# Kernel tuning notes

Measured on AMD Instinct MI355X. Metric: run time of the kernel, lower is better.

## Reference

```python
import jax, jax.numpy as jnp
import numpy as np

N, E, IN, H, O, K = 50000, 800000, 256, 128, 32, 5
ALPHA, EPS = 0.1, 1e-5


def setup_inputs() -> dict:
    key = jax.random.key(0)
    ks = jax.random.split(key, 20)
    nrm = lambda k, shape, s=0.02: jax.random.normal(k, shape, dtype=jnp.float32) * s
    H2 = H // 2
    return {
        "x": jax.random.normal(ks[0], (N, IN), dtype=jnp.float32),
        "edge_index": jax.random.randint(ks[1], (2, E), 0, N),
        "edge_weight": jax.random.uniform(ks[2], (E,), dtype=jnp.float32),
        # lin1 + bn1
        "W1": nrm(ks[3], (IN, H)), "b1": jnp.zeros((H,), jnp.float32),
        "g1": jnp.ones((H,), jnp.float32), "be1": jnp.zeros((H,), jnp.float32),
        "m1": nrm(ks[4], (H,), 0.1), "v1": 1.0 + 0.1 * jax.random.uniform(ks[5], (H,), dtype=jnp.float32),
        # lin2 + bn2
        "W2": nrm(ks[6], (H, H)), "b2": jnp.zeros((H,), jnp.float32),
        "g2": jnp.ones((H,), jnp.float32), "be2": jnp.zeros((H,), jnp.float32),
        "m2": nrm(ks[7], (H,), 0.1), "v2": 1.0 + 0.1 * jax.random.uniform(ks[8], (H,), dtype=jnp.float32),
        # attention over hop outputs (K+1)
        "att": jnp.ones((K + 1,), jnp.float32) + nrm(ks[9], (K + 1,), 0.1),
        # head: Linear(H, H//2) + BN + ReLU + Linear(H//2, O)
        "W3": nrm(ks[10], (H, H2)), "b3": jnp.zeros((H2,), jnp.float32),
        "g3": jnp.ones((H2,), jnp.float32), "be3": jnp.zeros((H2,), jnp.float32),
        "m3": nrm(ks[11], (H2,), 0.1), "v3": 1.0 + 0.1 * jax.random.uniform(ks[12], (H2,), dtype=jnp.float32),
        "W4": nrm(ks[13], (H2, O)), "b4": jnp.zeros((O,), jnp.float32),
    }


def _bn(t, g, b, m, v):
    # eval-mode BatchNorm1d using running stats
    return (t - m) * (g / jnp.sqrt(v + EPS)) + b


def reference(x, edge_index, edge_weight, W1, b1, g1, be1, m1, v1,
              W2, b2, g2, be2, m2, v2, att,
              W3, b3, g3, be3, m3, v3, W4, b4):
    n = x.shape[0]
    row, col = edge_index[0], edge_index[1]

    h = jax.nn.relu(_bn(x @ W1 + b1, g1, be1, m1, v1))
    identity = h
    h = jax.nn.relu(_bn(h @ W2 + b2, g2, be2, m2, v2)) + identity

    # weighted edge normalization: out-weight sum per source node, clamped >= 1
    wsum = jnp.maximum(jax.ops.segment_sum(edge_weight, row, num_segments=n), 1.0)
    edge_norm = edge_weight / wsum[row]  # [E]

    def prop(h_in):
        # APPNP-style: K inner iterations blending toward this call's h0
        h0 = h_in
        hk = h_in
        for _ in range(K):
            msg = hk[row] * edge_norm[:, None]          # [E, H] gather + scale
            agg = jax.ops.segment_sum(msg, col, num_segments=n)  # scatter-add
            hk = (1.0 - ALPHA) * agg + ALPHA * h0
        return hk

    xs = [h]
    hc = h
    for _ in range(K):  # outer loop: att has K+1 weights
        hc = prop(hc)
        xs.append(hc)

    stacked = jnp.stack(xs, axis=-1)          # [N, H, K+1]
    w = jax.nn.softmax(att)                   # [K+1]
    fused = jnp.einsum('nhk,k->nh', stacked, w)

    hid = jax.nn.relu(_bn(fused @ W3 + b3, g3, be3, m3, v3))
    return hid @ W4 + b4
```

## Files before the change

kernel.cpp:

```cpp
#include <hip/hip_runtime.h>
#include <cstddef>
#include <cstdint>

namespace {

constexpr int N   = 50000;
constexpr int E   = 800000;
constexpr int IN  = 256;
constexpr int H   = 128;
constexpr int H2v = 64;
constexpr int O   = 32;
constexpr int K   = 5;
constexpr float ALPHA = 0.1f;
constexpr float EPS   = 1e-5f;
constexpr int SCAN_CH = 1024;
constexpr int SCAN_NB = (N + SCAN_CH - 1) / SCAN_CH;
constexpr int NPAD = 50048;
constexpr int NPW  = 8;

typedef __bf16 bf16x8 __attribute__((ext_vector_type(8)));
typedef float  f32x4  __attribute__((ext_vector_type(4)));

__device__ inline uint32_t pack2_bf16(float x, float y) {
  uint32_t ux = __float_as_uint(x);
  uint32_t uy = __float_as_uint(y);
  ux = (ux + 0x7FFFu + ((ux >> 16) & 1u)) >> 16;
  uy = (uy + 0x7FFFu + ((uy >> 16) & 1u)) & 0xFFFF0000u;
  return uy | ux;
}
__device__ inline unsigned short bf16_1(float x) {
  uint32_t u = __float_as_uint(x);
  return (unsigned short)((u + 0x7FFFu + ((u >> 16) & 1u)) >> 16);
}
__device__ inline float bf16_lo(uint32_t v) { return __uint_as_float(v << 16); }
__device__ inline float bf16_hi(uint32_t v) { return __uint_as_float(v & 0xFFFF0000u); }
__device__ inline float bf16_f(unsigned short h) { return __uint_as_float(((uint32_t)h) << 16); }

__global__ void zero2_kernel(int* __restrict__ a, int* __restrict__ b, int n) {
  int i = blockIdx.x * blockDim.x + threadIdx.x;
  if (i < n) { a[i] = 0; b[i] = 0; }
}

__global__ void softmax_att_kernel(const float* __restrict__ att, float* __restrict__ wk) {
  if (threadIdx.x == 0 && blockIdx.x == 0) {
    float mx = att[0];
    for (int i = 1; i < K + 1; ++i) mx = fmaxf(mx, att[i]);
    float ex[K + 1];
    float s = 0.f;
    for (int i = 0; i < K + 1; ++i) { ex[i] = expf(att[i] - mx); s += ex[i]; }
    for (int i = 0; i < K + 1; ++i) wk[i] = ex[i] / s;
  }
}

__global__ void hist_kernel(const int* __restrict__ row, const int* __restrict__ col,
                            const float* __restrict__ ew,
                            int* __restrict__ deg, float* __restrict__ wsum) {
  int i = blockIdx.x * blockDim.x + threadIdx.x;
  if (i < E) {
    atomicAdd(&deg[col[i]], 1);
    atomicAdd(&wsum[row[i]], ew[i]);
  }
}

__global__ __launch_bounds__(256) void scan_local_kernel(const int* __restrict__ deg,
                                                         int* __restrict__ offs,
                                                         int* __restrict__ bsum) {
  __shared__ int sd[256];
  int base = blockIdx.x * SCAN_CH;
  int t = threadIdx.x;
  int v[4];
  int s = 0;
#pragma unroll
  for (int u = 0; u < 4; ++u) {
    int i = base + t * 4 + u;
    v[u] = (i < N) ? deg[i] : 0;
    s += v[u];
  }
  sd[t] = s;
  __syncthreads();
  int val = s;
  for (int off = 1; off < 256; off <<= 1) {
    int x = (t >= off) ? sd[t - off] : 0;
    __syncthreads();
    val += x;
    sd[t] = val;
    __syncthreads();
  }
  int excl = val - s;
#pragma unroll
  for (int u = 0; u < 4; ++u) {
    int i = base + t * 4 + u;
    if (i < N) offs[i] = excl;
    excl += v[u];
  }
  if (t == 255) bsum[blockIdx.x] = val;
}

__global__ void scan_bsum_kernel(int* __restrict__ bsum) {
  if (threadIdx.x == 0 && blockIdx.x == 0) {
    int acc = 0;
    for (int i = 0; i < SCAN_NB; ++i) {
      int v = bsum[i];
      bsum[i] = acc;
      acc += v;
    }
    bsum[SCAN_NB] = acc;
  }
}

__global__ void scan_add_kernel(int* __restrict__ offs, const int* __restrict__ bsum,
                                int* __restrict__ cursor) {
  int i = blockIdx.x * blockDim.x + threadIdx.x;
  if (i < N) {
    int o = offs[i] + bsum[i / SCAN_CH];
    offs[i] = o;
    cursor[i] = o;
  }
  if (i == 0) offs[N] = bsum[SCAN_NB];
}

__global__ void fill_kernel(const int* __restrict__ row, const int* __restrict__ col,
                            const float* __restrict__ ew, const float* __restrict__ wsum,
                            int* __restrict__ cursor, uint2* __restrict__ csr) {
  int i = blockIdx.x * blockDim.x + threadIdx.x;
  if (i < E) {
    int d = col[i];
    int p = atomicAdd(&cursor[d], 1);
    int s = row[i];
    float w = ew[i] / fmaxf(wsum[s], 1.0f);
    csr[p] = make_uint2((uint32_t)s, __float_as_uint(w));
  }
}

__global__ void conv_x_kernel(const float* __restrict__ x, unsigned short* __restrict__ xbf) {
  int i = blockIdx.x * blockDim.x + threadIdx.x;
  size_t base = (size_t)i * 8;
  int r = (int)(base / IN);
  uint4 pk = {0, 0, 0, 0};
  if (r < N) {
    float4 a = *(const float4*)&x[base];
    float4 b = *(const float4*)&x[base + 4];
    pk.x = pack2_bf16(a.x, a.y);
    pk.y = pack2_bf16(a.z, a.w);
    pk.z = pack2_bf16(b.x, b.y);
    pk.w = pack2_bf16(b.z, b.w);
  }
  *(uint4*)&xbf[base] = pk;
}

__global__ void conv_wt_kernel(const float* __restrict__ W, unsigned short* __restrict__ Wt,
                               int Kdim) {
  int t = blockIdx.x * blockDim.x + threadIdx.x;
  int k8 = Kdim / 8;
  int n = t / k8;
  int kk = (t % k8) * 8;
  if (n >= H) return;
  float f[8];
#pragma unroll
  for (int j = 0; j < 8; ++j) f[j] = W[(size_t)(kk + j) * H + n];
  uint4 pk;
  pk.x = pack2_bf16(f[0], f[1]);
  pk.y = pack2_bf16(f[2], f[3]);
  pk.z = pack2_bf16(f[4], f[5]);
  pk.w = pack2_bf16(f[6], f[7]);
  *(uint4*)&Wt[(size_t)n * Kdim + kk] = pk;
}

__global__ __launch_bounds__(256) void mlp1_mfma_kernel(
    const unsigned short* __restrict__ xbf, const unsigned short* __restrict__ Wt1,
    const float* __restrict__ b1, const float* __restrict__ g1,
    const float* __restrict__ be1, const float* __restrict__ m1,
    const float* __restrict__ v1, unsigned short* __restrict__ h1bf) {
  int wave = threadIdx.x >> 6;
  int lane = threadIdx.x & 63;
  int m_base = blockIdx.x * 64 + wave * 16;
  int idx16 = lane & 15;
  int quad = lane >> 4;
  bf16x8 afrag[8];
  const unsigned short* xrow = xbf + (size_t)(m_base + idx16) * IN + quad * 8;
#pragma unroll
  for (int k0 = 0; k0 < 8; ++k0) afrag[k0] = *(const bf16x8*)(xrow + k0 * 32);
#pragma unroll
  for (int n0 = 0; n0 < 8; ++n0) {
    f32x4 acc = {0.f, 0.f, 0.f, 0.f};
    const unsigned short* wrow = Wt1 + (size_t)(n0 * 16 + idx16) * IN + quad * 8;
#pragma unroll
    for (int k0 = 0; k0 < 8; ++k0) {
      bf16x8 bfrag = *(const bf16x8*)(wrow + k0 * 32);
      acc = __builtin_amdgcn_mfma_f32_16x16x32_bf16(afrag[k0], bfrag, acc, 0, 0, 0);
    }
    int n = n0 * 16 + idx16;
    float sc = g1[n] * rsqrtf(v1[n] + EPS);
    float ad = b1[n] - m1[n];
    float bb = be1[n];
#pragma unroll
    for (int r = 0; r < 4; ++r) {
      int m = m_base + quad * 4 + r;
      float val = fmaxf((acc[r] + ad) * sc + bb, 0.f);
      h1bf[(size_t)m * H + n] = bf16_1(val);
    }
  }
}

__global__ __launch_bounds__(256) void mlp2_mfma_kernel(
    const unsigned short* __restrict__ h1bf, const unsigned short* __restrict__ Wt2,
    const float* __restrict__ b2, const float* __restrict__ g2,
    const float* __restrict__ be2, const float* __restrict__ m2,
    const float* __restrict__ v2, unsigned short* __restrict__ h0bf,
    float* __restrict__ fused, const float* __restrict__ wk) {
  int wave = threadIdx.x >> 6;
  int lane = threadIdx.x & 63;
  int m_base = blockIdx.x * 64 + wave * 16;
  int idx16 = lane & 15;
  int quad = lane >> 4;
  bf16x8 afrag[4];
  const unsigned short* arow = h1bf + (size_t)(m_base + idx16) * H + quad * 8;
#pragma unroll
  for (int k0 = 0; k0 < 4; ++k0) afrag[k0] = *(const bf16x8*)(arow + k0 * 32);
  float w0 = wk[0];
#pragma unroll
  for (int n0 = 0; n0 < 8; ++n0) {
    f32x4 acc = {0.f, 0.f, 0.f, 0.f};
    const unsigned short* wrow = Wt2 + (size_t)(n0 * 16 + idx16) * H + quad * 8;
#pragma unroll
    for (int k0 = 0; k0 < 4; ++k0) {
      bf16x8 bfrag = *(const bf16x8*)(wrow + k0 * 32);
      acc = __builtin_amdgcn_mfma_f32_16x16x32_bf16(afrag[k0], bfrag, acc, 0, 0, 0);
    }
    int n = n0 * 16 + idx16;
    float sc = g2[n] * rsqrtf(v2[n] + EPS);
    float ad = b2[n] - m2[n];
    float bb = be2[n];
#pragma unroll
    for (int r = 0; r < 4; ++r) {
      int m = m_base + quad * 4 + r;
      if (m < N) {
        float idv = bf16_f(h1bf[(size_t)m * H + n]);
        float val = fmaxf((acc[r] + ad) * sc + bb, 0.f) + idv;
        h0bf[(size_t)m * H + n] = bf16_1(val);
        fused[(size_t)m * H + n] = w0 * val;
      }
    }
  }
}

__global__ __launch_bounds__(256) void prop_kernel(
    const unsigned short* __restrict__ hk, const unsigned short* __restrict__ h0,
    unsigned short* __restrict__ outb,
    const int* __restrict__ offs, const uint2* __restrict__ csr,
    float* __restrict__ fused, const float* __restrict__ wk, int wj) {
  int wave = threadIdx.x >> 6;
  int lane = threadIdx.x & 63;
  int node0 = (blockIdx.x * 4 + wave) * NPW;
  int c = lane * 2;
  float wj_w = (wj >= 0) ? wk[wj] : 0.f;
  for (int nn = 0; nn < NPW; ++nn) {
    int node = node0 + nn;
    if (node >= N) return;
    int beg = offs[node];
    int end = offs[node + 1];
    float ax = 0.f, ay = 0.f;
    int e = beg;
    for (; e + 8 <= end; e += 8) {
      uint2 ew[8];
#pragma unroll
      for (int u = 0; u < 8; ++u) ew[u] = csr[e + u];
      uint32_t v[8];
#pragma unroll
      for (int u = 0; u < 8; ++u) v[u] = *(const uint32_t*)&hk[(size_t)ew[u].x * H + c];
#pragma unroll
      for (int u = 0; u < 8; ++u) {
        float w = __uint_as_float(ew[u].y);
        ax += w * bf16_lo(v[u]);
        ay += w * bf16_hi(v[u]);
      }
    }
    for (; e + 4 <= end; e += 4) {
      uint2 ew[4];
#pragma unroll
      for (int u = 0; u < 4; ++u) ew[u] = csr[e + u];
      uint32_t v[4];
#pragma unroll
      for (int u = 0; u < 4; ++u) v[u] = *(const uint32_t*)&hk[(size_t)ew[u].x * H + c];
#pragma unroll
      for (int u = 0; u < 4; ++u) {
        float w = __uint_as_float(ew[u].y);
        ax += w * bf16_lo(v[u]);
        ay += w * bf16_hi(v[u]);
      }
    }
    for (; e < end; ++e) {
      uint2 ew = csr[e];
      float w = __uint_as_float(ew.y);
      uint32_t v = *(const uint32_t*)&hk[(size_t)ew.x * H + c];
      ax += w * bf16_lo(v);
      ay += w * bf16_hi(v);
    }
    size_t idx = (size_t)node * H + c;
    uint32_t hv = *(const uint32_t*)&h0[idx];
    float vx = (1.f - ALPHA) * ax + ALPHA * bf16_lo(hv);
    float vy = (1.f - ALPHA) * ay + ALPHA * bf16_hi(hv);
    *(uint32_t*)&outb[idx] = pack2_bf16(vx, vy);
    if (wj >= 0) {
      float2 f = *(float2*)&fused[idx];
      f.x += wj_w * vx;
      f.y += wj_w * vy;
      *(float2*)&fused[idx] = f;
    }
  }
}

__global__ __launch_bounds__(64) void head_kernel(
    const float* __restrict__ fused, const float* __restrict__ W3,
    const float* __restrict__ b3, const float* __restrict__ g3,
    const float* __restrict__ be3, const float* __restrict__ m3,
    const float* __restrict__ v3, const float* __restrict__ W4,
    const float* __restrict__ b4, float* __restrict__ out) {
  __shared__ float fl[16][H];
  __shared__ float hl[16][H2v];
  int node0 = blockIdx.x * 16;
  int t = threadIdx.x;
  for (int idx = t * 4; idx < 16 * H; idx += 64 * 4) {
    int r = idx >> 7, c = idx & (H - 1);
    *(float4*)&fl[r][c] = *(const float4*)&fused[(size_t)(node0 + r) * H + c];
  }
  __syncthreads();
  {
    int ng = t >> 4;
    int c0 = (t & 15) * 4;
    float acc[4][4];
#pragma unroll
    for (int a = 0; a < 4; ++a)
#pragma unroll
      for (int b = 0; b < 4; ++b) acc[a][b] = 0.f;
    for (int k = 0; k < H; k += 4) {
      float4 xv[4];
#pragma unroll
      for (int a = 0; a < 4; ++a) xv[a] = *(const float4*)&fl[ng * 4 + a][k];
      float4 wv[4];
#pragma unroll
      for (int j = 0; j < 4; ++j) wv[j] = *(const float4*)&W3[(size_t)(k + j) * H2v + c0];
#pragma unroll
      for (int a = 0; a < 4; ++a) {
        float xa0 = xv[a].x, xa1 = xv[a].y, xa2 = xv[a].z, xa3 = xv[a].w;
        acc[a][0] += xa0 * wv[0].x + xa1 * wv[1].x + xa2 * wv[2].x + xa3 * wv[3].x;
        acc[a][1] += xa0 * wv[0].y + xa1 * wv[1].y + xa2 * wv[2].y + xa3 * wv[3].y;
        acc[a][2] += xa0 * wv[0].z + xa1 * wv[1].z + xa2 * wv[2].z + xa3 * wv[3].z;
        acc[a][3] += xa0 * wv[0].w + xa1 * wv[1].w + xa2 * wv[2].w + xa3 * wv[3].w;
      }
    }
    float sc[4], ad[4], bb[4];
#pragma unroll
    for (int b = 0; b < 4; ++b) {
      int c = c0 + b;
      sc[b] = g3[c] * rsqrtf(v3[c] + EPS);
      ad[b] = b3[c] - m3[c];
      bb[b] = be3[c];
    }
#pragma unroll
    for (int a = 0; a < 4; ++a)
#pragma unroll
      for (int b = 0; b < 4; ++b)
        hl[ng * 4 + a][c0 + b] = fmaxf((acc[a][b] + ad[b]) * sc[b] + bb[b], 0.f);
  }
  __syncthreads();
  {
    int co = t & 31;
    int nh = t >> 5;
    float bias = b4[co];
#pragma unroll
    for (int a = 0; a < 8; ++a) {
      int nloc = nh * 8 + a;
      float accf = bias;
      for (int k = 0; k < H2v; k += 4) {
        float4 hv = *(const float4*)&hl[nloc][k];
        accf += hv.x * W4[(size_t)(k + 0) * O + co];
        accf += hv.y * W4[(size_t)(k + 1) * O + co];
        accf += hv.z * W4[(size_t)(k + 2) * O + co];
        accf += hv.w * W4[(size_t)(k + 3) * O + co];
      }
      out[(size_t)(node0 + nloc) * O + co] = accf;
    }
  }
}

}

extern "C" void kernel_launch(void* const* d_in, const int* in_sizes, int n_in,
                              void* d_out, int out_size, void* d_ws, size_t ws_size,
                              hipStream_t stream) {
  const float* x   = (const float*)d_in[0];
  const int*   ei  = (const int*)d_in[1];
  const float* ew  = (const float*)d_in[2];
  const float* W1  = (const float*)d_in[3];
  const float* b1  = (const float*)d_in[4];
  const float* g1  = (const float*)d_in[5];
  const float* be1 = (const float*)d_in[6];
  const float* m1  = (const float*)d_in[7];
  const float* v1  = (const float*)d_in[8];
  const float* W2  = (const float*)d_in[9];
  const float* b2  = (const float*)d_in[10];
  const float* g2  = (const float*)d_in[11];
  const float* be2 = (const float*)d_in[12];
  const float* m2  = (const float*)d_in[13];
  const float* v2  = (const float*)d_in[14];
  const float* att = (const float*)d_in[15];
  const float* W3  = (const float*)d_in[16];
  const float* b3  = (const float*)d_in[17];
  const float* g3  = (const float*)d_in[18];
  const float* be3 = (const float*)d_in[19];
  const float* m3  = (const float*)d_in[20];
  const float* v3  = (const float*)d_in[21];
  const float* W4  = (const float*)d_in[22];
  const float* b4  = (const float*)d_in[23];
  const int* row = ei;
  const int* col = ei + E;
  float* out = (float*)d_out;

  char* p = (char*)d_ws;
  auto carve = [&](size_t bytes) -> void* {
    void* q = (void*)p;
    p += (bytes + 255) & ~(size_t)255;
    return q;
  };
  int*   deg     = (int*)carve((size_t)N * 4);
  float* wsum    = (float*)carve((size_t)N * 4);
  int*   offs    = (int*)carve((size_t)(N + 1) * 4);
  int*   cursor  = (int*)carve((size_t)N * 4);
  int*   bsum    = (int*)carve((size_t)(SCAN_NB + 1) * 4);
  uint2* csr     = (uint2*)carve((size_t)E * 8);
  float* wk      = (float*)carve(64);
  unsigned short* xbf  = (unsigned short*)carve((size_t)NPAD * IN * 2);
  unsigned short* Wt1  = (unsigned short*)carve((size_t)H * IN * 2);
  unsigned short* Wt2  = (unsigned short*)carve((size_t)H * H * 2);
  unsigned short* h1bf = (unsigned short*)carve((size_t)NPAD * H * 2);
  unsigned short* bf0  = (unsigned short*)carve((size_t)N * H * 2);
  unsigned short* bfA  = (unsigned short*)carve((size_t)N * H * 2);
  unsigned short* bfB  = (unsigned short*)carve((size_t)N * H * 2);
  float* fused   = (float*)carve((size_t)N * H * 4);

  const int tb = 256;
  zero2_kernel<<<(N + tb - 1) / tb, tb, 0, stream>>>(deg, (int*)wsum, N);
  softmax_att_kernel<<<1, 64, 0, stream>>>(att, wk);
  hist_kernel<<<(E + tb - 1) / tb, tb, 0, stream>>>(row, col, ew, deg, wsum);
  scan_local_kernel<<<SCAN_NB, 256, 0, stream>>>(deg, offs, bsum);
  scan_bsum_kernel<<<1, 64, 0, stream>>>(bsum);
  scan_add_kernel<<<(N + tb - 1) / tb, tb, 0, stream>>>(offs, bsum, cursor);
  fill_kernel<<<(E + tb - 1) / tb, tb, 0, stream>>>(row, col, ew, wsum, cursor, csr);

  conv_x_kernel<<<(NPAD * IN / 8 + tb - 1) / tb, tb, 0, stream>>>(x, xbf);
  conv_wt_kernel<<<(H * (IN / 8) + tb - 1) / tb, tb, 0, stream>>>(W1, Wt1, IN);
  conv_wt_kernel<<<(H * (H / 8) + tb - 1) / tb, tb, 0, stream>>>(W2, Wt2, H);

  mlp1_mfma_kernel<<<NPAD / 64, 256, 0, stream>>>(xbf, Wt1, b1, g1, be1, m1, v1, h1bf);
  mlp2_mfma_kernel<<<NPAD / 64, 256, 0, stream>>>(h1bf, Wt2, b2, g2, be2, m2, v2,
                                                  bf0, fused, wk);

  unsigned short* h0 = bf0;
  unsigned short* pa = bfA;
  unsigned short* pb = bfB;
  const int prop_blocks = (N + 4 * NPW - 1) / (4 * NPW);
  for (int j = 1; j <= K; ++j) {
    const unsigned short* src = h0;
    unsigned short* dst = pa;
    for (int i = 0; i < K; ++i) {
      int wj = (i == K - 1) ? j : -1;
      prop_kernel<<<prop_blocks, 256, 0, stream>>>(src, h0, dst, offs, csr, fused, wk, wj);
      if (i < K - 1) {
        src = dst;
        dst = (dst == pa) ? pb : pa;
      }
    }
    unsigned short* oldh0 = h0;
    h0 = pa;
    pa = pb;
    pb = oldh0;
  }

  head_kernel<<<N / 16, 64, 0, stream>>>(fused, W3, b3, g3, be3, m3, v3, W4, b4, out);
}
```

Baseline: 1.323 ms.

## Split each wave into quarter-wave edge groups with 16-byte row gathers

The propagation kernel now splits each wave into four 16-lane quarters. Each quarter handles a different edge of the node at the same time and loads 8 bf16 features (16 bytes) per lane, instead of the whole wave walking edges one at a time with 4-byte loads. Partial sums are combined with cross-quarter shuffles, and one quarter writes the bf16 output while another updates the fused accumulator. The offsets and bf16 buffers are padded to NPAD so the per-node bounds check can go, and nodes per wave drop from 8 to 4. This adds shuffle and reduction overhead and idles lanes on low-degree tails, in exchange for more gathers in flight per wave.

```diff
diff --git a/kernel.cpp b/kernel.cpp
--- a/kernel.cpp
+++ b/kernel.cpp
@@ -16,7 +16,7 @@
 constexpr int SCAN_CH = 1024;
 constexpr int SCAN_NB = (N + SCAN_CH - 1) / SCAN_CH;
 constexpr int NPAD = 50048;
-constexpr int NPW  = 8;
+constexpr int NPW  = 4;
 
 typedef __bf16 bf16x8 __attribute__((ext_vector_type(8)));
 typedef float  f32x4  __attribute__((ext_vector_type(4)));
@@ -115,8 +115,9 @@
     int o = offs[i] + bsum[i / SCAN_CH];
     offs[i] = o;
     cursor[i] = o;
-  }
-  if (i == 0) offs[N] = bsum[SCAN_NB];
+  } else if (i <= NPAD) {
+    offs[i] = bsum[SCAN_NB];
+  }
 }
 
 __global__ void fill_kernel(const int* __restrict__ row, const int* __restrict__ col,
@@ -251,61 +252,94 @@
     float* __restrict__ fused, const float* __restrict__ wk, int wj) {
   int wave = threadIdx.x >> 6;
   int lane = threadIdx.x & 63;
+  int quarter = lane >> 4;
+  int colb = (lane & 15) * 8;
   int node0 = (blockIdx.x * 4 + wave) * NPW;
-  int c = lane * 2;
   float wj_w = (wj >= 0) ? wk[wj] : 0.f;
   for (int nn = 0; nn < NPW; ++nn) {
     int node = node0 + nn;
-    if (node >= N) return;
     int beg = offs[node];
     int end = offs[node + 1];
-    float ax = 0.f, ay = 0.f;
-    int e = beg;
-    for (; e + 8 <= end; e += 8) {
-      uint2 ew[8];
-#pragma unroll
-      for (int u = 0; u < 8; ++u) ew[u] = csr[e + u];
-      uint32_t v[8];
-#pragma unroll
-      for (int u = 0; u < 8; ++u) v[u] = *(const uint32_t*)&hk[(size_t)ew[u].x * H + c];
-#pragma unroll
-      for (int u = 0; u < 8; ++u) {
-        float w = __uint_as_float(ew[u].y);
-        ax += w * bf16_lo(v[u]);
-        ay += w * bf16_hi(v[u]);
+    int deg = end - beg;
+    float a[8];
+#pragma unroll
+    for (int j = 0; j < 8; ++j) a[j] = 0.f;
+    int nfull = deg >> 2;
+    int qi = 0;
+    for (; qi + 4 <= nfull; qi += 4) {
+      uint2 ce[4];
+      uint4 rv[4];
+#pragma unroll
+      for (int u = 0; u < 4; ++u) ce[u] = csr[beg + (qi + u) * 4 + quarter];
+#pragma unroll
+      for (int u = 0; u < 4; ++u) rv[u] = *(const uint4*)&hk[(size_t)ce[u].x * H + colb];
+#pragma unroll
+      for (int u = 0; u < 4; ++u) {
+        float w = __uint_as_float(ce[u].y);
+        a[0] += w * bf16_lo(rv[u].x); a[1] += w * bf16_hi(rv[u].x);
+        a[2] += w * bf16_lo(rv[u].y); a[3] += w * bf16_hi(rv[u].y);
+        a[4] += w * bf16_lo(rv[u].z); a[5] += w * bf16_hi(rv[u].z);
+        a[6] += w * bf16_lo(rv[u].w); a[7] += w * bf16_hi(rv[u].w);
       }
     }
-    for (; e + 4 <= end; e += 4) {
-      uint2 ew[4];
-#pragma unroll
-      for (int u = 0; u < 4; ++u) ew[u] = csr[e + u];
-      uint32_t v[4];
-#pragma unroll
-      for (int u = 0; u < 4; ++u) v[u] = *(const uint32_t*)&hk[(size_t)ew[u].x * H + c];
-#pragma unroll
-      for (int u = 0; u < 4; ++u) {
-        float w = __uint_as_float(ew[u].y);
-        ax += w * bf16_lo(v[u]);
-        ay += w * bf16_hi(v[u]);
-      }
-    }
-    for (; e < end; ++e) {
-      uint2 ew = csr[e];
-      float w = __uint_as_float(ew.y);
-      uint32_t v = *(const uint32_t*)&hk[(size_t)ew.x * H + c];
-      ax += w * bf16_lo(v);
-      ay += w * bf16_hi(v);
-    }
-    size_t idx = (size_t)node * H + c;
-    uint32_t hv = *(const uint32_t*)&h0[idx];
-    float vx = (1.f - ALPHA) * ax + ALPHA * bf16_lo(hv);
-    float vy = (1.f - ALPHA) * ay + ALPHA * bf16_hi(hv);
-    *(uint32_t*)&outb[idx] = pack2_bf16(vx, vy);
-    if (wj >= 0) {
-      float2 f = *(float2*)&fused[idx];
-      f.x += wj_w * vx;
-      f.y += wj_w * vy;
-      *(float2*)&fused[idx] = f;
+    for (; qi < nfull; ++qi) {
+      uint2 ce = csr[beg + qi * 4 + quarter];
+      uint4 rv = *(const uint4*)&hk[(size_t)ce.x * H + colb];
+      float w = __uint_as_float(ce.y);
+      a[0] += w * bf16_lo(rv.x); a[1] += w * bf16_hi(rv.x);
+      a[2] += w * bf16_lo(rv.y); a[3] += w * bf16_hi(rv.y);
+      a[4] += w * bf16_lo(rv.z); a[5] += w * bf16_hi(rv.z);
+      a[6] += w * bf16_lo(rv.w); a[7] += w * bf16_hi(rv.w);
+    }
+    if (deg & 3) {
+      int e = beg + nfull * 4 + quarter;
+      bool valid = e < end;
+      uint2 ce = csr[valid ? e : beg];
+      float w = valid ? __uint_as_float(ce.y) : 0.f;
+      uint4 rv = *(const uint4*)&hk[(size_t)ce.x * H + colb];
+      a[0] += w * bf16_lo(rv.x); a[1] += w * bf16_hi(rv.x);
+      a[2] += w * bf16_lo(rv.y); a[3] += w * bf16_hi(rv.y);
+      a[4] += w * bf16_lo(rv.z); a[5] += w * bf16_hi(rv.z);
+      a[6] += w * bf16_lo(rv.w); a[7] += w * bf16_hi(rv.w);
+    }
+#pragma unroll
+    for (int j = 0; j < 8; ++j) {
+      a[j] += __shfl_xor(a[j], 16, 64);
+      a[j] += __shfl_xor(a[j], 32, 64);
+    }
+    size_t idx = (size_t)node * H + colb;
+    if (quarter == 0) {
+      uint4 hv = *(const uint4*)&h0[idx];
+      float v0 = (1.f - ALPHA) * a[0] + ALPHA * bf16_lo(hv.x);
+      float v1 = (1.f - ALPHA) * a[1] + ALPHA * bf16_hi(hv.x);
+      float v2 = (1.f - ALPHA) * a[2] + ALPHA * bf16_lo(hv.y);
+      float v3 = (1.f - ALPHA) * a[3] + ALPHA * bf16_hi(hv.y);
+      float v4 = (1.f - ALPHA) * a[4] + ALPHA * bf16_lo(hv.z);
+      float v5 = (1.f - ALPHA) * a[5] + ALPHA * bf16_hi(hv.z);
+      float v6 = (1.f - ALPHA) * a[6] + ALPHA * bf16_lo(hv.w);
+      float v7 = (1.f - ALPHA) * a[7] + ALPHA * bf16_hi(hv.w);
+      uint4 pk;
+      pk.x = pack2_bf16(v0, v1);
+      pk.y = pack2_bf16(v2, v3);
+      pk.z = pack2_bf16(v4, v5);
+      pk.w = pack2_bf16(v6, v7);
+      *(uint4*)&outb[idx] = pk;
+    } else if (quarter == 1 && wj >= 0 && node < N) {
+      uint4 hv = *(const uint4*)&h0[idx];
+      float v0 = (1.f - ALPHA) * a[0] + ALPHA * bf16_lo(hv.x);
+      float v1 = (1.f - ALPHA) * a[1] + ALPHA * bf16_hi(hv.x);
+      float v2 = (1.f - ALPHA) * a[2] + ALPHA * bf16_lo(hv.y);
+      float v3 = (1.f - ALPHA) * a[3] + ALPHA * bf16_hi(hv.y);
+      float v4 = (1.f - ALPHA) * a[4] + ALPHA * bf16_lo(hv.z);
+      float v5 = (1.f - ALPHA) * a[5] + ALPHA * bf16_hi(hv.z);
+      float v6 = (1.f - ALPHA) * a[6] + ALPHA * bf16_lo(hv.w);
+      float v7 = (1.f - ALPHA) * a[7] + ALPHA * bf16_hi(hv.w);
+      float4 f0 = *(float4*)&fused[idx];
+      float4 f1 = *(float4*)&fused[idx + 4];
+      f0.x += wj_w * v0; f0.y += wj_w * v1; f0.z += wj_w * v2; f0.w += wj_w * v3;
+      f1.x += wj_w * v4; f1.y += wj_w * v5; f1.z += wj_w * v6; f1.w += wj_w * v7;
+      *(float4*)&fused[idx] = f0;
+      *(float4*)&fused[idx + 4] = f1;
     }
   }
 }
@@ -425,7 +459,7 @@
   };
   int*   deg     = (int*)carve((size_t)N * 4);
   float* wsum    = (float*)carve((size_t)N * 4);
-  int*   offs    = (int*)carve((size_t)(N + 1) * 4);
+  int*   offs    = (int*)carve((size_t)(NPAD + 1) * 4);
   int*   cursor  = (int*)carve((size_t)N * 4);
   int*   bsum    = (int*)carve((size_t)(SCAN_NB + 1) * 4);
   uint2* csr     = (uint2*)carve((size_t)E * 8);
@@ -434,9 +468,9 @@
   unsigned short* Wt1  = (unsigned short*)carve((size_t)H * IN * 2);
   unsigned short* Wt2  = (unsigned short*)carve((size_t)H * H * 2);
   unsigned short* h1bf = (unsigned short*)carve((size_t)NPAD * H * 2);
-  unsigned short* bf0  = (unsigned short*)carve((size_t)N * H * 2);
-  unsigned short* bfA  = (unsigned short*)carve((size_t)N * H * 2);
-  unsigned short* bfB  = (unsigned short*)carve((size_t)N * H * 2);
+  unsigned short* bf0  = (unsigned short*)carve((size_t)NPAD * H * 2);
+  unsigned short* bfA  = (unsigned short*)carve((size_t)NPAD * H * 2);
+  unsigned short* bfB  = (unsigned short*)carve((size_t)NPAD * H * 2);
   float* fused   = (float*)carve((size_t)N * H * 4);
 
   const int tb = 256;
@@ -445,7 +479,7 @@
   hist_kernel<<<(E + tb - 1) / tb, tb, 0, stream>>>(row, col, ew, deg, wsum);
   scan_local_kernel<<<SCAN_NB, 256, 0, stream>>>(deg, offs, bsum);
   scan_bsum_kernel<<<1, 64, 0, stream>>>(bsum);
-  scan_add_kernel<<<(N + tb - 1) / tb, tb, 0, stream>>>(offs, bsum, cursor);
+  scan_add_kernel<<<(NPAD + 1 + tb - 1) / tb, tb, 0, stream>>>(offs, bsum, cursor);
   fill_kernel<<<(E + tb - 1) / tb, tb, 0, stream>>>(row, col, ew, wsum, cursor, csr);
 
   conv_x_kernel<<<(NPAD * IN / 8 + tb - 1) / tb, tb, 0, stream>>>(x, xbf);
@@ -459,7 +493,7 @@
   unsigned short* h0 = bf0;
   unsigned short* pa = bfA;
   unsigned short* pb = bfB;
-  const int prop_blocks = (N + 4 * NPW - 1) / (4 * NPW);
+  const int prop_blocks = NPAD / (4 * NPW);
   for (int j = 1; j <= K; ++j) {
     const unsigned short* src = h0;
     unsigned short* dst = pa;
```

After: 1.269 ms. 1.04x faster.
